# Kernel tuning notes

Hardware: AMD Instinct MI355X
Metric: run time of the kernel (lower is better)

## Reference

```python
import jax, jax.numpy as jnp
import numpy as np

N_A, N_B = 30000, 30000
V, D_IN, D_OUT, H, E = 2, 128, 128, 4, 480000
EPS_LN = 1e-5


def setup_inputs() -> dict:
    key = jax.random.key(0)
    ks = jax.random.split(key, 22)
    rn = lambda i, sh, s=1.0: jax.random.normal(ks[i], sh, dtype=jnp.float32) * s
    ri = lambda i, n: jax.random.randint(ks[i], (E,), 0, n, dtype=jnp.int32)
    return {
        'feat_A': rn(0, (N_A, V, D_IN)),
        'feat_B': rn(1, (N_B, V, D_IN)),
        'src_ab': ri(2, N_A), 'dst_ab': ri(3, N_B),
        'val_ab': jax.random.uniform(ks[4], (E,), dtype=jnp.float32),
        'src_ba': ri(5, N_B), 'dst_ba': ri(6, N_A),
        'val_ba': jax.random.uniform(ks[7], (E,), dtype=jnp.float32),
        'W1': rn(8, (D_OUT, D_IN), 0.05), 'b1': jnp.zeros((D_OUT,), jnp.float32),
        'g1': jnp.ones((D_OUT,), jnp.float32), 'be1': jnp.zeros((D_OUT,), jnp.float32),
        'W2': rn(9, (D_OUT, D_IN), 0.05), 'b2': jnp.zeros((D_OUT,), jnp.float32),
        'g2': jnp.ones((D_OUT,), jnp.float32), 'be2': jnp.zeros((D_OUT,), jnp.float32),
        'Win': rn(10, (3 * D_OUT, D_OUT), 0.05), 'bin_': jnp.zeros((3 * D_OUT,), jnp.float32),
        'Wout': rn(11, (D_OUT, D_OUT), 0.05), 'bout': jnp.zeros((D_OUT,), jnp.float32),
        'lng': jnp.ones((D_OUT,), jnp.float32), 'lnb': jnp.zeros((D_OUT,), jnp.float32),
    }


def spmm_t(src, dst, val, h, n_out):
    # (adj^T @ h) over all views: h [N_src, V, d] -> [n_out, V, d]
    msg = h[src] * val[:, None, None]
    return jax.ops.segment_sum(msg, dst, num_segments=n_out)


def l2norm(x):
    n = jnp.sqrt(jnp.sum(x * x, axis=-1, keepdims=True))
    return x / jnp.maximum(n, 1e-12)


def layernorm(x, g, b):
    mu = jnp.mean(x, axis=-1, keepdims=True)
    var = jnp.mean((x - mu) ** 2, axis=-1, keepdims=True)
    return (x - mu) * jax.lax.rsqrt(var + EPS_LN) * g + b


def proj(x, W, b, g, be):
    # Linear -> LayerNorm -> ReLU
    return jax.nn.relu(layernorm(x @ W.T + b, g, be))


def mha(x, Win, bin_, Wout, bout, num_heads):
    # self-attention over the metapath axis P; x [..., P, d]
    *lead, P, d = x.shape
    dh = d // num_heads
    q, k, v = jnp.split(x @ Win.T + bin_, 3, axis=-1)
    hd = lambda t: t.reshape(*lead, P, num_heads, dh)
    q = hd(q) * (dh ** -0.5)
    scores = jnp.einsum('...qhe,...khe->...hqk', q, hd(k))
    a = jax.nn.softmax(scores, axis=-1)
    o = jnp.einsum('...hqk,...khe->...qhe', a, hd(v)).reshape(*lead, P, d)
    return o @ Wout.T + bout


def reference(feat_A, feat_B, src_ab, dst_ab, val_ab, src_ba, dst_ba, val_ba,
              W1, b1, g1, be1, W2, b2, g2, be2, Win, bin_, Wout, bout, lng, lnb):
    # metapath A->B->A
    h = l2norm(spmm_t(src_ab, dst_ab, val_ab, feat_A, N_B))
    h = l2norm(spmm_t(src_ba, dst_ba, val_ba, h, N_A))
    h1 = proj(h, W1, b1, g1, be1)                       # [N_A, V, d]
    # metapath B->A
    h = l2norm(spmm_t(src_ba, dst_ba, val_ba, feat_B, N_A))
    h2 = proj(h, W2, b2, g2, be2)                       # [N_A, V, d]
    x = jnp.stack([h1, h2], axis=2)                     # [N_A, V, P=2, d]
    attn = mha(x, Win, bin_, Wout, bout, H)
    y = layernorm(attn + x, lng, lnb).mean(axis=2)      # [N_A, V, d]
    return y  # h_global['A']; type B is identity passthrough of feat_B
```

## Files before the change

### kernel.cpp

```cpp
#include <hip/hip_runtime.h>

#define D 128
#define NODE_ROW 256
#define AP 8
#define AR (AP * 2)

typedef __attribute__((ext_vector_type(8))) short short8;
typedef __attribute__((ext_vector_type(4))) float floatx4;

__device__ __forceinline__ ushort f2bf(float f) {
    unsigned int u = __float_as_uint(f);
    u += 0x7fffu + ((u >> 16) & 1u);
    return (ushort)(u >> 16);
}
__device__ __forceinline__ unsigned int pk2(float a, float b) {
    return (unsigned int)f2bf(a) | ((unsigned int)f2bf(b) << 16);
}
__device__ __forceinline__ void up8(uint4 u, float* f) {
    f[0] = __uint_as_float(u.x << 16); f[1] = __uint_as_float(u.x & 0xffff0000u);
    f[2] = __uint_as_float(u.y << 16); f[3] = __uint_as_float(u.y & 0xffff0000u);
    f[4] = __uint_as_float(u.z << 16); f[5] = __uint_as_float(u.z & 0xffff0000u);
    f[6] = __uint_as_float(u.w << 16); f[7] = __uint_as_float(u.w & 0xffff0000u);
}
__device__ __forceinline__ float bf2f(ushort h) {
    return __uint_as_float(((unsigned int)h) << 16);
}
__device__ __forceinline__ short8 ldfrag(const ushort* p) {
    union { uint4 u; short8 s; } cv;
    cv.u = *(const uint4*)p;
    return cv.s;
}
__device__ __forceinline__ void acc4(float4& a, float w, uint2 u) {
    a.x += w * __uint_as_float(u.x << 16);
    a.y += w * __uint_as_float(u.x & 0xffff0000u);
    a.z += w * __uint_as_float(u.y << 16);
    a.w += w * __uint_as_float(u.y & 0xffff0000u);
}

__global__ __launch_bounds__(256) void k_f2b2(
    const float* __restrict__ srcA, const float* __restrict__ srcB,
    ushort* __restrict__ dstA, ushort* __restrict__ dstB, int n8) {
    int i = blockIdx.x * 256 + threadIdx.x;
    const float* s; ushort* d; int k;
    if (i < n8) { s = srcA; d = dstA; k = i; }
    else if (i < 2 * n8) { s = srcB; d = dstB; k = i - n8; }
    else return;
    const float4* sp = (const float4*)s + (size_t)k * 2;
    float4 a = sp[0], b = sp[1];
    uint4 o;
    o.x = pk2(a.x, a.y); o.y = pk2(a.z, a.w);
    o.z = pk2(b.x, b.y); o.w = pk2(b.z, b.w);
    ((uint4*)d)[k] = o;
}


__global__ __launch_bounds__(256) void k_hist(
    const int* __restrict__ dst_ab, const int* __restrict__ dst_ba,
    int* __restrict__ cnt_ab, int* __restrict__ cnt_ba, int E) {
    int i = blockIdx.x * 256 + threadIdx.x;
    if (i >= E) return;
    atomicAdd(&cnt_ab[dst_ab[i]], 1);
    atomicAdd(&cnt_ba[dst_ba[i]], 1);
}

__global__ __launch_bounds__(1024) void k_scan2(
    int* __restrict__ cntB, int* __restrict__ startB, int nB_,
    int* __restrict__ cntA, int* __restrict__ startA, int nA_) {
    __shared__ int part[1024];
    int* cnt; int* start; int n;
    if (blockIdx.x == 0) { cnt = cntB; start = startB; n = nB_; }
    else                 { cnt = cntA; start = startA; n = nA_; }
    int t = threadIdx.x;
    int chunk = (n + 1023) >> 10;
    int lo = min(t * chunk, n), hi = min(lo + chunk, n);
    int s = 0;
    for (int i = lo; i < hi; i++) s += cnt[i];
    part[t] = s;
    __syncthreads();
    for (int d = 1; d < 1024; d <<= 1) {
        int v = (t >= d) ? part[t - d] : 0;
        __syncthreads();
        part[t] += v;
        __syncthreads();
    }
    int off = part[t] - s;
    for (int i = lo; i < hi; i++) {
        int c = cnt[i];
        start[i] = off;
        cnt[i] = off;
        off += c;
    }
    if (t == 1023) start[n] = off;
}

__global__ __launch_bounds__(256) void k_scatter(
    const int* __restrict__ src_ab, const int* __restrict__ dst_ab,
    const float* __restrict__ val_ab,
    const int* __restrict__ src_ba, const int* __restrict__ dst_ba,
    const float* __restrict__ val_ba,
    int* __restrict__ cur_ab, int* __restrict__ cur_ba,
    int2* __restrict__ ep_ab, int2* __restrict__ ep_ba, int E) {
    int i = blockIdx.x * 256 + threadIdx.x;
    if (i >= E) return;
    {
        int pos = atomicAdd(&cur_ab[dst_ab[i]], 1);
        ep_ab[pos] = make_int2(src_ab[i], __float_as_int(val_ab[i]));
    }
    {
        int pos = atomicAdd(&cur_ba[dst_ba[i]], 1);
        ep_ba[pos] = make_int2(src_ba[i], __float_as_int(val_ba[i]));
    }
}


__global__ __launch_bounds__(256) void k_gather_norm_bf(
    const ushort* __restrict__ feat, const int2* __restrict__ ep,
    const int* __restrict__ start, ushort* __restrict__ out, int n) {
    int node = blockIdx.x * 4 + (threadIdx.x >> 6);
    if (node >= n) return;
    int lane = threadIdx.x & 63;
    int lo = start[node], hi = start[node + 1];
    float4 acc = make_float4(0.f, 0.f, 0.f, 0.f);
    int i = lo;
    for (; i + 3 < hi; i += 4) {
        int2 p0 = ep[i], p1 = ep[i + 1], p2 = ep[i + 2], p3 = ep[i + 3];
        uint2 u0 = ((const uint2*)(feat + (size_t)p0.x * NODE_ROW))[lane];
        uint2 u1 = ((const uint2*)(feat + (size_t)p1.x * NODE_ROW))[lane];
        uint2 u2 = ((const uint2*)(feat + (size_t)p2.x * NODE_ROW))[lane];
        uint2 u3 = ((const uint2*)(feat + (size_t)p3.x * NODE_ROW))[lane];
        acc4(acc, __int_as_float(p0.y), u0);
        acc4(acc, __int_as_float(p1.y), u1);
        acc4(acc, __int_as_float(p2.y), u2);
        acc4(acc, __int_as_float(p3.y), u3);
    }
    for (; i < hi; i++) {
        int2 p = ep[i];
        uint2 u = ((const uint2*)(feat + (size_t)p.x * NODE_ROW))[lane];
        acc4(acc, __int_as_float(p.y), u);
    }
    float ss = acc.x * acc.x + acc.y * acc.y + acc.z * acc.z + acc.w * acc.w;
    #pragma unroll
    for (int o = 16; o > 0; o >>= 1) ss += __shfl_xor(ss, o, 32);
    float sc = 1.0f / fmaxf(sqrtf(ss), 1e-12f);
    uint2 o;
    o.x = pk2(acc.x * sc, acc.y * sc);
    o.y = pk2(acc.z * sc, acc.w * sc);
    ((uint2*)(out + (size_t)node * NODE_ROW))[lane] = o;
}

__global__ __launch_bounds__(256) void k_gather2_bf(
    const ushort* __restrict__ featP, const ushort* __restrict__ featQ,
    const int2* __restrict__ ep, const int* __restrict__ start,
    ushort* __restrict__ outP, ushort* __restrict__ outQ, int n) {
    int node = blockIdx.x * 4 + (threadIdx.x >> 6);
    if (node >= n) return;
    int lane = threadIdx.x & 63;
    int lo = start[node], hi = start[node + 1];
    float4 aP = make_float4(0.f, 0.f, 0.f, 0.f);
    float4 aQ = make_float4(0.f, 0.f, 0.f, 0.f);
    int i = lo;
    for (; i + 3 < hi; i += 4) {
        int2 p0 = ep[i], p1 = ep[i + 1], p2 = ep[i + 2], p3 = ep[i + 3];
        size_t o0 = (size_t)p0.x * NODE_ROW, o1 = (size_t)p1.x * NODE_ROW;
        size_t o2 = (size_t)p2.x * NODE_ROW, o3 = (size_t)p3.x * NODE_ROW;
        uint2 uP0 = ((const uint2*)(featP + o0))[lane];
        uint2 uQ0 = ((const uint2*)(featQ + o0))[lane];
        uint2 uP1 = ((const uint2*)(featP + o1))[lane];
        uint2 uQ1 = ((const uint2*)(featQ + o1))[lane];
        uint2 uP2 = ((const uint2*)(featP + o2))[lane];
        uint2 uQ2 = ((const uint2*)(featQ + o2))[lane];
        uint2 uP3 = ((const uint2*)(featP + o3))[lane];
        uint2 uQ3 = ((const uint2*)(featQ + o3))[lane];
        float w0 = __int_as_float(p0.y), w1 = __int_as_float(p1.y);
        float w2 = __int_as_float(p2.y), w3 = __int_as_float(p3.y);
        acc4(aP, w0, uP0); acc4(aQ, w0, uQ0);
        acc4(aP, w1, uP1); acc4(aQ, w1, uQ1);
        acc4(aP, w2, uP2); acc4(aQ, w2, uQ2);
        acc4(aP, w3, uP3); acc4(aQ, w3, uQ3);
    }
    for (; i < hi; i++) {
        int2 p = ep[i];
        float w = __int_as_float(p.y);
        size_t off = (size_t)p.x * NODE_ROW;
        uint2 uP = ((const uint2*)(featP + off))[lane];
        uint2 uQ = ((const uint2*)(featQ + off))[lane];
        acc4(aP, w, uP); acc4(aQ, w, uQ);
    }
    uint2 oP, oQ;
    oP.x = pk2(aP.x, aP.y); oP.y = pk2(aP.z, aP.w);
    oQ.x = pk2(aQ.x, aQ.y); oQ.y = pk2(aQ.z, aQ.w);
    ((uint2*)(outP + (size_t)node * NODE_ROW))[lane] = oP;
    ((uint2*)(outQ + (size_t)node * NODE_ROW))[lane] = oQ;
}

__global__ __launch_bounds__(256) void k_cvt(
    const float* __restrict__ W1, const float* __restrict__ W2,
    const float* __restrict__ Win, const float* __restrict__ Wout,
    ushort* __restrict__ dst) {
    int idx = (blockIdx.x * 256 + threadIdx.x) * 4;
    if (idx >= 98304) return;
    const float* s; int off;
    if (idx < 16384)      { s = W1;  off = idx; }
    else if (idx < 32768) { s = W2;  off = idx - 16384; }
    else if (idx < 81920) { s = Win; off = idx - 32768; }
    else                  { s = Wout; off = idx - 81920; }
    float4 f = *(const float4*)(s + off);
    uint2 p;
    p.x = pk2(f.x, f.y);
    p.y = pk2(f.z, f.w);
    *(uint2*)(dst + idx) = p;
}

__global__ __launch_bounds__(128) void k_projm2(
    const ushort* __restrict__ in1, const ushort* __restrict__ Wb1,
    const float* __restrict__ b1, const float* __restrict__ g1,
    const float* __restrict__ be1,
    const ushort* __restrict__ in2, const ushort* __restrict__ Wb2,
    const float* __restrict__ b2, const float* __restrict__ g2,
    const float* __restrict__ be2,
    ushort* __restrict__ xbuf) {
    __shared__ ushort xn[16][136];
    __shared__ float yb[16][128];
    int p = blockIdx.y;
    const ushort* in = p ? in2 : in1;
    const ushort* Wb = p ? Wb2 : Wb1;
    const float*  b  = p ? b2  : b1;
    const float*  g  = p ? g2  : g1;
    const float*  be = p ? be2 : be1;
    int t = threadIdx.x;
    size_t rowbase = (size_t)blockIdx.x * 16;
    int r = t >> 3, i = t & 7;

    {
        const ushort* gp = in + (rowbase + r) * D + i * 16;
        float v[16];
        up8(((const uint4*)gp)[0], v);
        up8(((const uint4*)gp)[1], v + 8);
        float ss = 0.f;
        #pragma unroll
        for (int e = 0; e < 16; e++) ss += v[e] * v[e];
        ss += __shfl_xor(ss, 1, 8);
        ss += __shfl_xor(ss, 2, 8);
        ss += __shfl_xor(ss, 4, 8);
        float sc = 1.0f / fmaxf(sqrtf(ss), 1e-12f);
        uint4 w0, w1;
        w0.x = pk2(v[0]*sc, v[1]*sc);   w0.y = pk2(v[2]*sc, v[3]*sc);
        w0.z = pk2(v[4]*sc, v[5]*sc);   w0.w = pk2(v[6]*sc, v[7]*sc);
        w1.x = pk2(v[8]*sc, v[9]*sc);   w1.y = pk2(v[10]*sc, v[11]*sc);
        w1.z = pk2(v[12]*sc, v[13]*sc); w1.w = pk2(v[14]*sc, v[15]*sc);
        ushort* dst = &xn[r][i * 16];
        ((uint4*)dst)[0] = w0;
        ((uint4*)dst)[1] = w1;
    }
    __syncthreads();

    {
        int lane = t & 63, w = t >> 6, c = lane & 15, quad = lane >> 4;
        short8 af[4];
        #pragma unroll
        for (int kt = 0; kt < 4; kt++)
            af[kt] = ldfrag(&xn[c][kt * 32 + quad * 8]);
        #pragma unroll
        for (int nt2 = 0; nt2 < 4; nt2++) {
            int j = (w * 4 + nt2) * 16 + c;
            floatx4 acc = {0.f, 0.f, 0.f, 0.f};
            #pragma unroll
            for (int kt = 0; kt < 4; kt++) {
                short8 bfr = ldfrag(Wb + (size_t)j * 128 + kt * 32 + quad * 8);
                acc = __builtin_amdgcn_mfma_f32_16x16x32_bf16(af[kt], bfr, acc, 0, 0, 0);
            }
            float bj = b[j];
            #pragma unroll
            for (int rg = 0; rg < 4; rg++)
                yb[quad * 4 + rg][j] = acc[rg] + bj;
        }
    }
    __syncthreads();

    {
        float v[16];
        const float* yr = &yb[r][i * 16];
        #pragma unroll
        for (int e = 0; e < 16; e++) v[e] = yr[e];
        float s1 = 0.f, s2 = 0.f;
        #pragma unroll
        for (int e = 0; e < 16; e++) { s1 += v[e]; s2 += v[e] * v[e]; }
        s1 += __shfl_xor(s1, 1, 8); s2 += __shfl_xor(s2, 1, 8);
        s1 += __shfl_xor(s1, 2, 8); s2 += __shfl_xor(s2, 2, 8);
        s1 += __shfl_xor(s1, 4, 8); s2 += __shfl_xor(s2, 4, 8);
        float mu = s1 * (1.0f / 128.0f);
        float var = s2 * (1.0f / 128.0f) - mu * mu;
        float rs = rsqrtf(var + 1e-5f);
        const float* gg = g + i * 16;
        const float* bb = be + i * 16;
        float res[16];
        #pragma unroll
        for (int e = 0; e < 16; e++)
            res[e] = fmaxf((v[e] - mu) * rs * gg[e] + bb[e], 0.f);
        ushort* op = xbuf + ((rowbase + r) * 2 + p) * D + i * 16;
        uint4 w0, w1;
        w0.x = pk2(res[0], res[1]);   w0.y = pk2(res[2], res[3]);
        w0.z = pk2(res[4], res[5]);   w0.w = pk2(res[6], res[7]);
        w1.x = pk2(res[8], res[9]);   w1.y = pk2(res[10], res[11]);
        w1.z = pk2(res[12], res[13]); w1.w = pk2(res[14], res[15]);
        ((uint4*)op)[0] = w0;
        ((uint4*)op)[1] = w1;
    }
}

__global__ __launch_bounds__(256, 6) void k_attn2(
    const ushort* __restrict__ xbuf,
    const ushort* __restrict__ Winb, const float* __restrict__ binq,
    const ushort* __restrict__ Woutb, const float* __restrict__ bout,
    const float* __restrict__ lng, const float* __restrict__ lnb,
    float* __restrict__ out) {
    __shared__ ushort xb[AR][136];
    __shared__ ushort obuf[AR][140];
    __shared__ float yy[AR][132];
    __shared__ float mu_s[AR], rs_s[AR];
    int t = threadIdx.x;
    int lane = t & 63, w = t >> 6;
    int c = lane & 15, quad = lane >> 4;
    size_t pairbase = (size_t)blockIdx.x * AP;
    size_t rowbase = pairbase * 2;

    const uint2* gx = (const uint2*)(xbuf + rowbase * D);
    #pragma unroll
    for (int i = t; i < AR * D / 4; i += 256) {
        int r = i >> 5;
        int col = (i & 31) * 4;
        *(uint2*)&xb[r][col] = gx[i];
    }
    __syncthreads();

    {
        short8 af[4];
        #pragma unroll
        for (int kt = 0; kt < 4; kt++)
            af[kt] = ldfrag(&xb[c][kt * 32 + quad * 8]);
        floatx4 aq0 = {0.f,0.f,0.f,0.f}, aq1 = {0.f,0.f,0.f,0.f};
        floatx4 ak0 = {0.f,0.f,0.f,0.f}, ak1 = {0.f,0.f,0.f,0.f};
        floatx4 av0 = {0.f,0.f,0.f,0.f}, av1 = {0.f,0.f,0.f,0.f};
        int jb = w * 32 + c;
        #pragma unroll
        for (int kt = 0; kt < 4; kt++) {
            const ushort* wp = Winb + kt * 32 + quad * 8;
            short8 f0 = ldfrag(wp + (size_t)(jb)       * 128);
            short8 f1 = ldfrag(wp + (size_t)(jb + 16)  * 128);
            short8 f2 = ldfrag(wp + (size_t)(jb + 128) * 128);
            short8 f3 = ldfrag(wp + (size_t)(jb + 144) * 128);
            short8 f4 = ldfrag(wp + (size_t)(jb + 256) * 128);
            short8 f5 = ldfrag(wp + (size_t)(jb + 272) * 128);
            aq0 = __builtin_amdgcn_mfma_f32_16x16x32_bf16(af[kt], f0, aq0, 0, 0, 0);
            aq1 = __builtin_amdgcn_mfma_f32_16x16x32_bf16(af[kt], f1, aq1, 0, 0, 0);
            ak0 = __builtin_amdgcn_mfma_f32_16x16x32_bf16(af[kt], f2, ak0, 0, 0, 0);
            ak1 = __builtin_amdgcn_mfma_f32_16x16x32_bf16(af[kt], f3, ak1, 0, 0, 0);
            av0 = __builtin_amdgcn_mfma_f32_16x16x32_bf16(af[kt], f4, av0, 0, 0, 0);
            av1 = __builtin_amdgcn_mfma_f32_16x16x32_bf16(af[kt], f5, av1, 0, 0, 0);
        }
        const float qs = 0.17677669529663687f;
        float bq0 = binq[jb] ;        float bq1 = binq[jb + 16];
        float bk0 = binq[jb + 128];   float bk1 = binq[jb + 144];
        float bv0 = binq[jb + 256];   float bv1 = binq[jb + 272];
        #pragma unroll
        for (int rg = 0; rg < 4; rg++) {
            aq0[rg] = (aq0[rg] + bq0) * qs;
            aq1[rg] = (aq1[rg] + bq1) * qs;
            ak0[rg] += bk0;  ak1[rg] += bk1;
            av0[rg] += bv0;  av1[rg] += bv1;
        }
        #pragma unroll
        for (int pl = 0; pl < 2; pl++) {
            int r0 = 2 * pl, r1 = 2 * pl + 1;
            float p00 = aq0[r0] * ak0[r0] + aq1[r0] * ak1[r0];
            float p01 = aq0[r0] * ak0[r1] + aq1[r0] * ak1[r1];
            float p10 = aq0[r1] * ak0[r0] + aq1[r1] * ak1[r0];
            float p11 = aq0[r1] * ak0[r1] + aq1[r1] * ak1[r1];
            #pragma unroll
            for (int m = 1; m < 16; m <<= 1) {
                p00 += __shfl_xor(p00, m, 16);
                p01 += __shfl_xor(p01, m, 16);
                p10 += __shfl_xor(p10, m, 16);
                p11 += __shfl_xor(p11, m, 16);
            }
            float mx0 = fmaxf(p00, p01), mx1 = fmaxf(p10, p11);
            float e00 = __expf(p00 - mx0), e01 = __expf(p01 - mx0);
            float e10 = __expf(p10 - mx1), e11 = __expf(p11 - mx1);
            float i0 = 1.f / (e00 + e01), i1 = 1.f / (e10 + e11);
            float a00 = e00 * i0, a01 = e01 * i0;
            float a10 = e10 * i1, a11 = e11 * i1;
            float o00 = a00 * av0[r0] + a01 * av0[r1];
            float o10 = a10 * av0[r0] + a11 * av0[r1];
            float o01 = a00 * av1[r0] + a01 * av1[r1];
            float o11 = a10 * av1[r0] + a11 * av1[r1];
            int row0 = quad * 4 + r0, row1 = quad * 4 + r1;
            obuf[row0][jb]      = f2bf(o00);
            obuf[row1][jb]      = f2bf(o10);
            obuf[row0][jb + 16] = f2bf(o01);
            obuf[row1][jb + 16] = f2bf(o11);
        }
    }
    __syncthreads();

    {
        short8 af[4];
        #pragma unroll
        for (int kt = 0; kt < 4; kt++)
            af[kt] = ldfrag(&obuf[c][kt * 32 + quad * 8]);
        #pragma unroll
        for (int nt2 = 0; nt2 < 2; nt2++) {
            int j = (w * 2 + nt2) * 16 + c;
            floatx4 acc = {0.f, 0.f, 0.f, 0.f};
            #pragma unroll
            for (int kt = 0; kt < 4; kt++) {
                short8 bfr = ldfrag(Woutb + (size_t)j * 128 + kt * 32 + quad * 8);
                acc = __builtin_amdgcn_mfma_f32_16x16x32_bf16(af[kt], bfr, acc, 0, 0, 0);
            }
            float bj = bout[j];
            #pragma unroll
            for (int rg = 0; rg < 4; rg++) {
                int row = quad * 4 + rg;
                yy[row][j] = acc[rg] + bj + bf2f(xb[row][j]);
            }
        }
    }
    __syncthreads();

    if (t < 128) {
        int r = t >> 3, i = t & 7;
        float s1 = 0.f, s2 = 0.f;
        const float* yr = &yy[r][i * 16];
        #pragma unroll
        for (int cc = 0; cc < 16; cc++) { float v = yr[cc]; s1 += v; s2 += v * v; }
        s1 += __shfl_down(s1, 4, 8); s2 += __shfl_down(s2, 4, 8);
        s1 += __shfl_down(s1, 2, 8); s2 += __shfl_down(s2, 2, 8);
        s1 += __shfl_down(s1, 1, 8); s2 += __shfl_down(s2, 1, 8);
        if (i == 0) {
            float mu = s1 / D;
            float var = s2 / D - mu * mu;
            mu_s[r] = mu; rs_s[r] = rsqrtf(var + 1e-5f);
        }
    }
    __syncthreads();

    if (t < 128) {
        int j = t;
        float gj = lng[j], bj = lnb[j];
        #pragma unroll
        for (int pp = 0; pp < AP; pp++) {
            int r0 = pp * 2, r1 = r0 + 1;
            float v0 = (yy[r0][j] - mu_s[r0]) * rs_s[r0] * gj + bj;
            float v1 = (yy[r1][j] - mu_s[r1]) * rs_s[r1] * gj + bj;
            out[(pairbase + pp) * D + j] = 0.5f * (v0 + v1);
        }
    }
}

extern "C" void kernel_launch(void* const* d_in, const int* in_sizes, int n_in,
                              void* d_out, int out_size, void* d_ws, size_t ws_size,
                              hipStream_t stream) {
    const float* feat_A = (const float*)d_in[0];
    const float* feat_B = (const float*)d_in[1];
    const int*   src_ab = (const int*)d_in[2];
    const int*   dst_ab = (const int*)d_in[3];
    const float* val_ab = (const float*)d_in[4];
    const int*   src_ba = (const int*)d_in[5];
    const int*   dst_ba = (const int*)d_in[6];
    const float* val_ba = (const float*)d_in[7];
    const float* W1 = (const float*)d_in[8];
    const float* b1 = (const float*)d_in[9];
    const float* g1 = (const float*)d_in[10];
    const float* be1 = (const float*)d_in[11];
    const float* W2 = (const float*)d_in[12];
    const float* b2 = (const float*)d_in[13];
    const float* g2 = (const float*)d_in[14];
    const float* be2 = (const float*)d_in[15];
    const float* Win = (const float*)d_in[16];
    const float* binq = (const float*)d_in[17];
    const float* Wout = (const float*)d_in[18];
    const float* bout = (const float*)d_in[19];
    const float* lng = (const float*)d_in[20];
    const float* lnb = (const float*)d_in[21];

    int E  = in_sizes[2];
    int nA = in_sizes[0] / NODE_ROW;
    int nB = in_sizes[1] / NODE_ROW;
    int rowsA = nA * 2;
    size_t nodeElems = (size_t)nA * NODE_ROW;

    ushort* fbA  = (ushort*)d_ws;
    ushort* fbB  = fbA + nodeElems;
    ushort* hB   = fbB + nodeElems;
    ushort* hA1  = hB + nodeElems;
    ushort* hA2  = hA1 + nodeElems;
    ushort* xbuf = hA2 + nodeElems;
    ushort* Wbf  = xbuf + (size_t)rowsA * 2 * D;
    ushort* W1b   = Wbf;
    ushort* W2b   = Wbf + 16384;
    ushort* Winb  = Wbf + 32768;
    ushort* Woutb = Wbf + 81920;
    int* cnt_ab   = (int*)(Wbf + 98304);
    int* cnt_ba   = cnt_ab + nB;
    int* start_ab = cnt_ba + nA;
    int* start_ba = start_ab + (nB + 1);
    uintptr_t a = (uintptr_t)(start_ba + (nA + 1));
    a = (a + 15) & ~(uintptr_t)15;
    int2* ep_ab = (int2*)a;
    int2* ep_ba = ep_ab + E;

    int egrid = (E + 255) / 256;
    int n8 = (int)(nodeElems / 8);

    k_f2b2<<<(2 * n8 + 255) / 256, 256, 0, stream>>>(feat_A, feat_B, fbA, fbB, n8);

    hipMemsetAsync(cnt_ab, 0, (size_t)(nA + nB) * sizeof(int), stream);
    k_hist<<<egrid, 256, 0, stream>>>(dst_ab, dst_ba, cnt_ab, cnt_ba, E);
    k_scan2<<<2, 1024, 0, stream>>>(cnt_ab, start_ab, nB, cnt_ba, start_ba, nA);
    k_scatter<<<egrid, 256, 0, stream>>>(src_ab, dst_ab, val_ab,
                                         src_ba, dst_ba, val_ba,
                                         cnt_ab, cnt_ba, ep_ab, ep_ba, E);

    k_cvt<<<96, 256, 0, stream>>>(W1, W2, Win, Wout, Wbf);

    k_gather_norm_bf<<<(nB + 3) / 4, 256, 0, stream>>>(fbA, ep_ab, start_ab, hB, nB);
    k_gather2_bf<<<(nA + 3) / 4, 256, 0, stream>>>(hB, fbB, ep_ba, start_ba,
                                                   hA1, hA2, nA);

    k_projm2<<<dim3(rowsA / 16, 2), 128, 0, stream>>>(hA1, W1b, b1, g1, be1,
                                                      hA2, W2b, b2, g2, be2, xbuf);
    k_attn2<<<rowsA / AP, 256, 0, stream>>>(xbuf, Winb, binq, Woutb, bout,
                                            lng, lnb, (float*)d_out);
}
```

Baseline: 567.9 us.

## Double attention tile per block and fuse LayerNorm stats into register epilogue

The attention kernel now handles 16 node pairs per block (two 16-row MFMA halves), so each Win/Wout fragment load is reused twice. It also drops the shared fp32 staging of the output-projection result. Each lane keeps its y values in registers, reduces sum and sum-of-squares with lane shuffles plus a small shared table, and applies LayerNorm and the pair mean directly. This removes shared-memory traffic and one barrier phase, at the cost of more registers and half as many blocks. The launch grid must halve to match the doubled AP, and that code is not shown.

```diff
diff --git a/kernel.cpp b/kernel.cpp
--- a/kernel.cpp
+++ b/kernel.cpp
@@ -2,7 +2,7 @@
 
 #define D 128
 #define NODE_ROW 256
-#define AP 8
+#define AP 16
 #define AR (AP * 2)
 
 typedef __attribute__((ext_vector_type(8))) short short8;
@@ -316,8 +316,7 @@
     float* __restrict__ out) {
     __shared__ ushort xb[AR][136];
     __shared__ ushort obuf[AR][140];
-    __shared__ float yy[AR][132];
-    __shared__ float mu_s[AR], rs_s[AR];
+    __shared__ float st[AR][12];
     int t = threadIdx.x;
     int lane = t & 63, w = t >> 6;
     int c = lane & 15, quad = lane >> 4;
@@ -333,125 +332,153 @@
     }
     __syncthreads();
 
-    {
-        short8 af[4];
-        #pragma unroll
-        for (int kt = 0; kt < 4; kt++)
-            af[kt] = ldfrag(&xb[c][kt * 32 + quad * 8]);
-        floatx4 aq0 = {0.f,0.f,0.f,0.f}, aq1 = {0.f,0.f,0.f,0.f};
-        floatx4 ak0 = {0.f,0.f,0.f,0.f}, ak1 = {0.f,0.f,0.f,0.f};
-        floatx4 av0 = {0.f,0.f,0.f,0.f}, av1 = {0.f,0.f,0.f,0.f};
-        int jb = w * 32 + c;
-        #pragma unroll
-        for (int kt = 0; kt < 4; kt++) {
-            const ushort* wp = Winb + kt * 32 + quad * 8;
-            short8 f0 = ldfrag(wp + (size_t)(jb)       * 128);
-            short8 f1 = ldfrag(wp + (size_t)(jb + 16)  * 128);
-            short8 f2 = ldfrag(wp + (size_t)(jb + 128) * 128);
-            short8 f3 = ldfrag(wp + (size_t)(jb + 144) * 128);
-            short8 f4 = ldfrag(wp + (size_t)(jb + 256) * 128);
-            short8 f5 = ldfrag(wp + (size_t)(jb + 272) * 128);
-            aq0 = __builtin_amdgcn_mfma_f32_16x16x32_bf16(af[kt], f0, aq0, 0, 0, 0);
-            aq1 = __builtin_amdgcn_mfma_f32_16x16x32_bf16(af[kt], f1, aq1, 0, 0, 0);
-            ak0 = __builtin_amdgcn_mfma_f32_16x16x32_bf16(af[kt], f2, ak0, 0, 0, 0);
-            ak1 = __builtin_amdgcn_mfma_f32_16x16x32_bf16(af[kt], f3, ak1, 0, 0, 0);
-            av0 = __builtin_amdgcn_mfma_f32_16x16x32_bf16(af[kt], f4, av0, 0, 0, 0);
-            av1 = __builtin_amdgcn_mfma_f32_16x16x32_bf16(af[kt], f5, av1, 0, 0, 0);
-        }
+    int jb = w * 32 + c;
+    {
         const float qs = 0.17677669529663687f;
-        float bq0 = binq[jb] ;        float bq1 = binq[jb + 16];
+        float bq0 = binq[jb];         float bq1 = binq[jb + 16];
         float bk0 = binq[jb + 128];   float bk1 = binq[jb + 144];
         float bv0 = binq[jb + 256];   float bv1 = binq[jb + 272];
         #pragma unroll
-        for (int rg = 0; rg < 4; rg++) {
-            aq0[rg] = (aq0[rg] + bq0) * qs;
-            aq1[rg] = (aq1[rg] + bq1) * qs;
-            ak0[rg] += bk0;  ak1[rg] += bk1;
-            av0[rg] += bv0;  av1[rg] += bv1;
+        for (int hf = 0; hf < 2; hf++) {
+            int rb = hf * 16;
+            short8 af[4];
+            #pragma unroll
+            for (int kt = 0; kt < 4; kt++)
+                af[kt] = ldfrag(&xb[rb + c][kt * 32 + quad * 8]);
+            floatx4 aq0 = {0.f,0.f,0.f,0.f}, aq1 = {0.f,0.f,0.f,0.f};
+            floatx4 ak0 = {0.f,0.f,0.f,0.f}, ak1 = {0.f,0.f,0.f,0.f};
+            floatx4 av0 = {0.f,0.f,0.f,0.f}, av1 = {0.f,0.f,0.f,0.f};
+            #pragma unroll
+            for (int kt = 0; kt < 4; kt++) {
+                const ushort* wp = Winb + kt * 32 + quad * 8;
+                short8 f0 = ldfrag(wp + (size_t)(jb)       * 128);
+                short8 f1 = ldfrag(wp + (size_t)(jb + 16)  * 128);
+                short8 f2 = ldfrag(wp + (size_t)(jb + 128) * 128);
+                short8 f3 = ldfrag(wp + (size_t)(jb + 144) * 128);
+                short8 f4 = ldfrag(wp + (size_t)(jb + 256) * 128);
+                short8 f5 = ldfrag(wp + (size_t)(jb + 272) * 128);
+                aq0 = __builtin_amdgcn_mfma_f32_16x16x32_bf16(af[kt], f0, aq0, 0, 0, 0);
+                aq1 = __builtin_amdgcn_mfma_f32_16x16x32_bf16(af[kt], f1, aq1, 0, 0, 0);
+                ak0 = __builtin_amdgcn_mfma_f32_16x16x32_bf16(af[kt], f2, ak0, 0, 0, 0);
+                ak1 = __builtin_amdgcn_mfma_f32_16x16x32_bf16(af[kt], f3, ak1, 0, 0, 0);
+                av0 = __builtin_amdgcn_mfma_f32_16x16x32_bf16(af[kt], f4, av0, 0, 0, 0);
+                av1 = __builtin_amdgcn_mfma_f32_16x16x32_bf16(af[kt], f5, av1, 0, 0, 0);
+            }
+            #pragma unroll
+            for (int rg = 0; rg < 4; rg++) {
+                aq0[rg] = (aq0[rg] + bq0) * qs;
+                aq1[rg] = (aq1[rg] + bq1) * qs;
+                ak0[rg] += bk0;  ak1[rg] += bk1;
+                av0[rg] += bv0;  av1[rg] += bv1;
+            }
+            #pragma unroll
+            for (int pl = 0; pl < 2; pl++) {
+                int r0 = 2 * pl, r1 = 2 * pl + 1;
+                float p00 = aq0[r0] * ak0[r0] + aq1[r0] * ak1[r0];
+                float p01 = aq0[r0] * ak0[r1] + aq1[r0] * ak1[r1];
+                float p10 = aq0[r1] * ak0[r0] + aq1[r1] * ak1[r0];
+                float p11 = aq0[r1] * ak0[r1] + aq1[r1] * ak1[r1];
+                #pragma unroll
+                for (int m = 1; m < 16; m <<= 1) {
+                    p00 += __shfl_xor(p00, m, 16);
+                    p01 += __shfl_xor(p01, m, 16);
+                    p10 += __shfl_xor(p10, m, 16);
+                    p11 += __shfl_xor(p11, m, 16);
+                }
+                float mx0 = fmaxf(p00, p01), mx1 = fmaxf(p10, p11);
+                float e00 = __expf(p00 - mx0), e01 = __expf(p01 - mx0);
+                float e10 = __expf(p10 - mx1), e11 = __expf(p11 - mx1);
+                float i0 = 1.f / (e00 + e01), i1 = 1.f / (e10 + e11);
+                float a00 = e00 * i0, a01 = e01 * i0;
+                float a10 = e10 * i1, a11 = e11 * i1;
+                float o00 = a00 * av0[r0] + a01 * av0[r1];
+                float o10 = a10 * av0[r0] + a11 * av0[r1];
+                float o01 = a00 * av1[r0] + a01 * av1[r1];
+                float o11 = a10 * av1[r0] + a11 * av1[r1];
+                int row0 = rb + quad * 4 + r0, row1 = rb + quad * 4 + r1;
+                obuf[row0][jb]      = f2bf(o00);
+                obuf[row1][jb]      = f2bf(o10);
+                obuf[row0][jb + 16] = f2bf(o01);
+                obuf[row1][jb + 16] = f2bf(o11);
+            }
         }
-        #pragma unroll
-        for (int pl = 0; pl < 2; pl++) {
-            int r0 = 2 * pl, r1 = 2 * pl + 1;
-            float p00 = aq0[r0] * ak0[r0] + aq1[r0] * ak1[r0];
-            float p01 = aq0[r0] * ak0[r1] + aq1[r0] * ak1[r1];
-            float p10 = aq0[r1] * ak0[r0] + aq1[r1] * ak1[r0];
-            float p11 = aq0[r1] * ak0[r1] + aq1[r1] * ak1[r1];
-            #pragma unroll
-            for (int m = 1; m < 16; m <<= 1) {
-                p00 += __shfl_xor(p00, m, 16);
-                p01 += __shfl_xor(p01, m, 16);
-                p10 += __shfl_xor(p10, m, 16);
-                p11 += __shfl_xor(p11, m, 16);
-            }
-            float mx0 = fmaxf(p00, p01), mx1 = fmaxf(p10, p11);
-            float e00 = __expf(p00 - mx0), e01 = __expf(p01 - mx0);
-            float e10 = __expf(p10 - mx1), e11 = __expf(p11 - mx1);
-            float i0 = 1.f / (e00 + e01), i1 = 1.f / (e10 + e11);
-            float a00 = e00 * i0, a01 = e01 * i0;
-            float a10 = e10 * i1, a11 = e11 * i1;
-            float o00 = a00 * av0[r0] + a01 * av0[r1];
-            float o10 = a10 * av0[r0] + a11 * av0[r1];
-            float o01 = a00 * av1[r0] + a01 * av1[r1];
-            float o11 = a10 * av1[r0] + a11 * av1[r1];
-            int row0 = quad * 4 + r0, row1 = quad * 4 + r1;
-            obuf[row0][jb]      = f2bf(o00);
-            obuf[row1][jb]      = f2bf(o10);
-            obuf[row0][jb + 16] = f2bf(o01);
-            obuf[row1][jb + 16] = f2bf(o11);
+    }
+    __syncthreads();
+
+    float y[2][2][4];
+    {
+        float bo0 = bout[jb], bo1 = bout[jb + 16];
+        #pragma unroll
+        for (int hf = 0; hf < 2; hf++) {
+            int rb = hf * 16;
+            short8 af[4];
+            #pragma unroll
+            for (int kt = 0; kt < 4; kt++)
+                af[kt] = ldfrag(&obuf[rb + c][kt * 32 + quad * 8]);
+            #pragma unroll
+            for (int nt2 = 0; nt2 < 2; nt2++) {
+                int j = jb + nt2 * 16;
+                floatx4 acc = {0.f, 0.f, 0.f, 0.f};
+                #pragma unroll
+                for (int kt = 0; kt < 4; kt++) {
+                    short8 bfr = ldfrag(Woutb + (size_t)j * 128 + kt * 32 + quad * 8);
+                    acc = __builtin_amdgcn_mfma_f32_16x16x32_bf16(af[kt], bfr, acc, 0, 0, 0);
+                }
+                float bj = nt2 ? bo1 : bo0;
+                #pragma unroll
+                for (int rg = 0; rg < 4; rg++)
+                    y[hf][nt2][rg] = acc[rg] + bj + bf2f(xb[rb + quad * 4 + rg][j]);
+            }
+            #pragma unroll
+            for (int rg = 0; rg < 4; rg++) {
+                float v0 = y[hf][0][rg], v1 = y[hf][1][rg];
+                float s1 = v0 + v1, s2 = v0 * v0 + v1 * v1;
+                #pragma unroll
+                for (int m = 1; m < 16; m <<= 1) {
+                    s1 += __shfl_xor(s1, m, 16);
+                    s2 += __shfl_xor(s2, m, 16);
+                }
+                if (c == 0) {
+                    st[rb + quad * 4 + rg][w * 2]     = s1;
+                    st[rb + quad * 4 + rg][w * 2 + 1] = s2;
+                }
+            }
         }
     }
     __syncthreads();
 
     {
-        short8 af[4];
-        #pragma unroll
-        for (int kt = 0; kt < 4; kt++)
-            af[kt] = ldfrag(&obuf[c][kt * 32 + quad * 8]);
-        #pragma unroll
-        for (int nt2 = 0; nt2 < 2; nt2++) {
-            int j = (w * 2 + nt2) * 16 + c;
-            floatx4 acc = {0.f, 0.f, 0.f, 0.f};
-            #pragma unroll
-            for (int kt = 0; kt < 4; kt++) {
-                short8 bfr = ldfrag(Woutb + (size_t)j * 128 + kt * 32 + quad * 8);
-                acc = __builtin_amdgcn_mfma_f32_16x16x32_bf16(af[kt], bfr, acc, 0, 0, 0);
-            }
-            float bj = bout[j];
-            #pragma unroll
-            for (int rg = 0; rg < 4; rg++) {
-                int row = quad * 4 + rg;
-                yy[row][j] = acc[rg] + bj + bf2f(xb[row][j]);
-            }
-        }
-    }
-    __syncthreads();
-
-    if (t < 128) {
-        int r = t >> 3, i = t & 7;
-        float s1 = 0.f, s2 = 0.f;
-        const float* yr = &yy[r][i * 16];
-        #pragma unroll
-        for (int cc = 0; cc < 16; cc++) { float v = yr[cc]; s1 += v; s2 += v * v; }
-        s1 += __shfl_down(s1, 4, 8); s2 += __shfl_down(s2, 4, 8);
-        s1 += __shfl_down(s1, 2, 8); s2 += __shfl_down(s2, 2, 8);
-        s1 += __shfl_down(s1, 1, 8); s2 += __shfl_down(s2, 1, 8);
-        if (i == 0) {
-            float mu = s1 / D;
-            float var = s2 / D - mu * mu;
-            mu_s[r] = mu; rs_s[r] = rsqrtf(var + 1e-5f);
-        }
-    }
-    __syncthreads();
-
-    if (t < 128) {
-        int j = t;
-        float gj = lng[j], bj = lnb[j];
-        #pragma unroll
-        for (int pp = 0; pp < AP; pp++) {
-            int r0 = pp * 2, r1 = r0 + 1;
-            float v0 = (yy[r0][j] - mu_s[r0]) * rs_s[r0] * gj + bj;
-            float v1 = (yy[r1][j] - mu_s[r1]) * rs_s[r1] * gj + bj;
-            out[(pairbase + pp) * D + j] = 0.5f * (v0 + v1);
+        float gj0 = lng[jb], gj1 = lng[jb + 16];
+        float bn0 = lnb[jb], bn1 = lnb[jb + 16];
+        #pragma unroll
+        for (int hf = 0; hf < 2; hf++) {
+            int rb = hf * 16;
+            #pragma unroll
+            for (int pl = 0; pl < 2; pl++) {
+                int rg0 = 2 * pl, rg1 = 2 * pl + 1;
+                int rl0 = rb + quad * 4 + rg0, rl1 = rl0 + 1;
+                float4 a0 = *(const float4*)&st[rl0][0];
+                float4 b0 = *(const float4*)&st[rl0][4];
+                float4 a1 = *(const float4*)&st[rl1][0];
+                float4 b1 = *(const float4*)&st[rl1][4];
+                float s10 = a0.x + a0.z + b0.x + b0.z;
+                float s20 = a0.y + a0.w + b0.y + b0.w;
+                float s11 = a1.x + a1.z + b1.x + b1.z;
+                float s21 = a1.y + a1.w + b1.y + b1.w;
+                float mu0 = s10 * (1.0f / 128.0f);
+                float var0 = s20 * (1.0f / 128.0f) - mu0 * mu0;
+                float rs0 = rsqrtf(var0 + 1e-5f);
+                float mu1 = s11 * (1.0f / 128.0f);
+                float var1 = s21 * (1.0f / 128.0f) - mu1 * mu1;
+                float rs1 = rsqrtf(var1 + 1e-5f);
+                float w00 = (y[hf][0][rg0] - mu0) * rs0 * gj0 + bn0;
+                float w01 = (y[hf][1][rg0] - mu0) * rs0 * gj1 + bn1;
+                float w10 = (y[hf][0][rg1] - mu1) * rs1 * gj0 + bn0;
+                float w11 = (y[hf][1][rg1] - mu1) * rs1 * gj1 + bn1;
+                size_t orow = pairbase + hf * 8 + quad * 2 + pl;
+                out[orow * D + jb]      = 0.5f * (w00 + w10);
+                out[orow * D + jb + 16] = 0.5f * (w01 + w11);
+            }
         }
     }
 }
```

Measured after the change: 577.8 us. No clear change (+1.7%).
